# Optimization experiments

Measured on AMD Instinct MI355X. Metric: run time of the kernel, lower is better.

Reference implementation:

```python
import jax, jax.numpy as jnp
import numpy as np

B = 2048          # batch
K = 32            # max active features per side
NF = 22528        # feature_set.num_features
L1 = 2048
L2 = 16
L3 = 32
P = 8             # num_psqt_buckets
NLS = 8           # num_ls_buckets
QP = 255.0        # 8-bit unsigned LSQ upper bound


def setup_inputs() -> dict:
    key = jax.random.key(0)
    ks = jax.random.split(key, 16)
    us = jax.random.bernoulli(ks[0], 0.5, (B, 1)).astype(jnp.float32)
    them = 1.0 - us
    white_indices = jax.random.randint(ks[1], (B, K), 0, NF)
    black_indices = jax.random.randint(ks[2], (B, K), 0, NF)
    white_values = jnp.ones((B, K), jnp.float32)
    black_values = jnp.ones((B, K), jnp.float32)
    psqt_indices = jax.random.randint(ks[3], (B,), 0, P)
    layer_stack_indices = jax.random.randint(ks[4], (B,), 0, NLS)
    # parameters
    ft_weight = jax.random.normal(ks[5], (NF, L1 + P), jnp.float32) * 0.01
    ft_bias = jax.random.normal(ks[6], (L1 + P,), jnp.float32) * 0.01
    lsq_s = jnp.full((4,), 1.0 / 128.0, jnp.float32)  # per-group step size
    W1 = jax.random.normal(ks[7], (NLS, L2, L1), jnp.float32) * (1.0 / np.sqrt(L1))
    b1 = jnp.zeros((NLS, L2), jnp.float32)
    W2 = jax.random.normal(ks[8], (NLS, L3, L2), jnp.float32) * (1.0 / np.sqrt(L2))
    b2 = jnp.zeros((NLS, L3), jnp.float32)
    Wo = jax.random.normal(ks[9], (NLS, 1, L3), jnp.float32) * (1.0 / np.sqrt(L3))
    bo = jnp.zeros((NLS, 1), jnp.float32)
    return dict(us=us, them=them, white_indices=white_indices, white_values=white_values,
                black_indices=black_indices, black_values=black_values,
                psqt_indices=psqt_indices, layer_stack_indices=layer_stack_indices,
                ft_weight=ft_weight, ft_bias=ft_bias, lsq_s=lsq_s,
                W1=W1, b1=b1, W2=W2, b2=b2, Wo=Wo, bo=bo)


def _feature_transform(idx, val, ft_weight, ft_bias):
    # sparse accumulation: sum_k val[b,k] * ft_weight[idx[b,k], :]
    emb = ft_weight[idx]                           # [B, K, L1+P]
    return jnp.einsum('bk,bkd->bd', val, emb) + ft_bias


def _lsq(x, s):
    # LSQ activation, 4 groups over feature dim, 8-bit unsigned, STE round
    b, d = x.shape
    g = x.reshape(b, 4, d // 4) / s[None, :, None]
    gc = jnp.clip(g, 0.0, QP)
    gq = gc + jax.lax.stop_gradient(jnp.round(gc) - gc)
    return (gq * s[None, :, None]).reshape(b, d)


def reference(us, them, white_indices, white_values, black_indices, black_values,
              psqt_indices, layer_stack_indices,
              ft_weight, ft_bias, lsq_s, W1, b1, W2, b2, Wo, bo):
    wp = _feature_transform(white_indices, white_values, ft_weight, ft_bias)
    bp = _feature_transform(black_indices, black_values, ft_weight, ft_bias)
    w, wpsqt = wp[:, :L1], wp[:, L1:]
    b, bpsqt = bp[:, :L1], bp[:, L1:]
    l0 = us * jnp.concatenate([w, b], axis=1) + them * jnp.concatenate([b, w], axis=1)
    l0q = _lsq(l0, lsq_s)                          # [B, 2*L1]
    s0, s1, s2, s3 = jnp.split(l0q, 4, axis=1)
    l0_mixed = jnp.concatenate([s0 * s1, s2 * s3], axis=1)   # [B, L1]
    # psqt bucket gather
    wps = jnp.take_along_axis(wpsqt, psqt_indices[:, None], axis=1)  # [B,1]
    bps = jnp.take_along_axis(bpsqt, psqt_indices[:, None], axis=1)
    # per-sample layer-stack (expert) selection
    i = layer_stack_indices
    h1 = jnp.clip(jnp.einsum('bi,boi->bo', l0_mixed, W1[i]) + b1[i], 0.0, 1.0)
    h2 = jnp.clip(jnp.einsum('bi,boi->bo', h1, W2[i]) + b2[i], 0.0, 1.0)
    ls_out = jnp.einsum('bi,boi->bo', h2, Wo[i]) + bo[i]     # [B,1]
    return ls_out + (wps - bps) * (us - 0.5)
```

## Files before the change

### kernel.cpp

```cpp
#include <hip/hip_runtime.h>

#define BB 2048
#define K 32
#define ROW 2056
#define L1D 2048
#define NT 512
#define NFEAT 22528
#define TBL_ELEMS ((size_t)NFEAT * ROW)
#define W1_ELEMS  ((size_t)8 * 16 * L1D)
#define TBL_BYTES (TBL_ELEMS * 2)
#define W1_OFF    TBL_BYTES
#define WS_NEEDED (TBL_BYTES + W1_ELEMS * 2)

__device__ __forceinline__ float bf2f(unsigned short s) {
    union { unsigned int u; float f; } v; v.u = ((unsigned int)s) << 16; return v.f;
}

__device__ __forceinline__ unsigned short f2bf(float f) {
    union { float f; unsigned int u; } v; v.f = f;
    const unsigned int u = v.u;
    return (unsigned short)((u + 0x7fffu + ((u >> 16) & 1u)) >> 16);
}

__device__ __forceinline__ void fma4(float4& a, float v, const float4 t) {
    a.x = fmaf(v, t.x, a.x); a.y = fmaf(v, t.y, a.y);
    a.z = fmaf(v, t.z, a.z); a.w = fmaf(v, t.w, a.w);
}

__device__ __forceinline__ void fma4u(float4& a, float v, const ushort4 t) {
    a.x = fmaf(v, bf2f(t.x), a.x); a.y = fmaf(v, bf2f(t.y), a.y);
    a.z = fmaf(v, bf2f(t.z), a.z); a.w = fmaf(v, bf2f(t.w), a.w);
}

__device__ __forceinline__ float4 add4(float4 a, float4 b) {
    float4 r; r.x = a.x + b.x; r.y = a.y + b.y; r.z = a.z + b.z; r.w = a.w + b.w;
    return r;
}

__device__ __forceinline__ float4 mix4(float ua, float4 a, float ub, float4 b) {
    float4 r;
    r.x = fmaf(ua, a.x, ub * b.x); r.y = fmaf(ua, a.y, ub * b.y);
    r.z = fmaf(ua, a.z, ub * b.z); r.w = fmaf(ua, a.w, ub * b.w);
    return r;
}

__device__ __forceinline__ float lsq1(float g, float s) {
    return rintf(fminf(fmaxf(g / s, 0.f), 255.f)) * s;
}

__device__ __forceinline__ float4 lsq4(float4 g, float s) {
    float4 r;
    r.x = lsq1(g.x, s); r.y = lsq1(g.y, s); r.z = lsq1(g.z, s); r.w = lsq1(g.w, s);
    return r;
}

__device__ __forceinline__ float4 mul4(float4 a, float4 b) {
    float4 r; r.x = a.x * b.x; r.y = a.y * b.y; r.z = a.z * b.z; r.w = a.w * b.w;
    return r;
}

__global__ __launch_bounds__(256) void conv_bf16(const float* __restrict__ src,
                                                 unsigned short* __restrict__ dst,
                                                 int n4) {
    int i = blockIdx.x * 256 + threadIdx.x;
    const int stride = gridDim.x * 256;
    for (; i < n4; i += stride) {
        const float4 v = ((const float4*)src)[i];
        ushort4 o;
        o.x = f2bf(v.x); o.y = f2bf(v.y); o.z = f2bf(v.z); o.w = f2bf(v.w);
        ((ushort4*)dst)[i] = o;
    }
}

__global__ __launch_bounds__(NT, 8) void nnue_fwd_bf16(
    const float* __restrict__ us_p,
    const float* __restrict__ them_p,
    const int*   __restrict__ widx,
    const float* __restrict__ wval,
    const int*   __restrict__ bidx,
    const float* __restrict__ bval,
    const int*   __restrict__ psqt_idx,
    const int*   __restrict__ ls_idx,
    const unsigned short* __restrict__ tbl,
    const float* __restrict__ ftb,
    const float* __restrict__ lsq_s,
    const unsigned short* __restrict__ w1bf,
    const float* __restrict__ b1,
    const float* __restrict__ W2,
    const float* __restrict__ b2,
    const float* __restrict__ Wo,
    const float* __restrict__ bo,
    float* __restrict__ out)
{
    const int b = blockIdx.x;
    const int t = threadIdx.x;

    __shared__ float4 sQA[NT];
    __shared__ float4 sQB[NT];
    __shared__ float4 sM[NT];
    __shared__ float  sH1t[16];
    __shared__ float  sH1[16];
    __shared__ float  sH2[32];
    __shared__ float  sPsq;

    const float usv = us_p[b];
    const float thv = them_p[b];

    float4 aw = {0,0,0,0}, ab = {0,0,0,0};
    #pragma unroll 4
    for (int k = 0; k < K; ++k) {
        const int   iw = widx[b * K + k];
        const float vw = wval[b * K + k];
        const int   ib = bidx[b * K + k];
        const float vb = bval[b * K + k];
        const ushort4 uw = ((const ushort4*)(tbl + (size_t)iw * ROW))[t];
        const ushort4 ub = ((const ushort4*)(tbl + (size_t)ib * ROW))[t];
        fma4u(aw, vw, uw);
        fma4u(ab, vb, ub);
    }

    const int pi = psqt_idx[b];
    if (t < 64) {
        const int k = t & 31;
        const int   idx = (t < 32) ? widx[b * K + k] : bidx[b * K + k];
        const float val = (t < 32) ? wval[b * K + k] : bval[b * K + k];
        float c = val * bf2f(tbl[(size_t)idx * ROW + 2048 + pi]);
        c += __shfl_down(c, 16, 32); c += __shfl_down(c, 8, 32);
        c += __shfl_down(c, 4, 32);  c += __shfl_down(c, 2, 32);
        c += __shfl_down(c, 1, 32);
        const float bsum = __shfl(c, 32);
        if (t == 0) sPsq = (c - bsum) * (usv - 0.5f);
    }

    const float s0 = lsq_s[0], s1 = lsq_s[1], s2 = lsq_s[2], s3 = lsq_s[3];
    const float4 bias = ((const float4*)ftb)[t];
    aw = add4(aw, bias);
    ab = add4(ab, bias);
    const float sA = (t < 256) ? s0 : s1;
    const float sB = (t < 256) ? s2 : s3;
    sQA[t] = lsq4(mix4(usv, aw, thv, ab), sA);
    sQB[t] = lsq4(mix4(usv, ab, thv, aw), sB);
    __syncthreads();

    if (t < 256) {
        sM[t]       = mul4(sQA[t], sQA[t + 256]);
        sM[t + 256] = mul4(sQB[t], sQB[t + 256]);
    }
    __syncthreads();

    const int i = ls_idx[b];
    const unsigned short* W1i = w1bf + (size_t)i * 16 * L1D;
    {
        const int o   = t >> 5;
        const int sub = t & 31;
        const ushort4* Wrow = (const ushort4*)(W1i + o * L1D);
        float4 a4 = {0,0,0,0};
        #pragma unroll
        for (int jj = 0; jj < 16; ++jj) {
            const int j4 = sub + (jj << 5);
            const float4  m = sM[j4];
            const ushort4 w = Wrow[j4];
            a4.x = fmaf(m.x, bf2f(w.x), a4.x); a4.y = fmaf(m.y, bf2f(w.y), a4.y);
            a4.z = fmaf(m.z, bf2f(w.z), a4.z); a4.w = fmaf(m.w, bf2f(w.w), a4.w);
        }
        float acc = (a4.x + a4.y) + (a4.z + a4.w);
        acc += __shfl_down(acc, 16, 32); acc += __shfl_down(acc, 8, 32);
        acc += __shfl_down(acc, 4, 32);  acc += __shfl_down(acc, 2, 32);
        acc += __shfl_down(acc, 1, 32);
        if (sub == 0) sH1t[o] = acc;
    }
    __syncthreads();

    if (t < 16) {
        const float v = sH1t[t] + b1[i * 16 + t];
        sH1[t] = fminf(fmaxf(v, 0.f), 1.f);
    }
    __syncthreads();

    if (t < 32) {
        const float* W2i = W2 + (size_t)i * 32 * 16 + t * 16;
        float v = b2[i * 32 + t];
        #pragma unroll
        for (int j = 0; j < 16; ++j) v = fmaf(sH1[j], W2i[j], v);
        sH2[t] = fminf(fmaxf(v, 0.f), 1.f);
    }
    __syncthreads();

    if (t == 0) {
        const float* Woi = Wo + (size_t)i * 32;
        float v = bo[i];
        #pragma unroll
        for (int j = 0; j < 32; ++j) v = fmaf(sH2[j], Woi[j], v);
        out[b] = v + sPsq;
    }
}

__global__ __launch_bounds__(NT, 8) void nnue_fwd_f32(
    const float* __restrict__ us_p, const float* __restrict__ them_p,
    const int* __restrict__ widx, const float* __restrict__ wval,
    const int* __restrict__ bidx, const float* __restrict__ bval,
    const int* __restrict__ psqt_idx, const int* __restrict__ ls_idx,
    const float* __restrict__ ftw, const float* __restrict__ ftb,
    const float* __restrict__ lsq_s, const float* __restrict__ W1,
    const float* __restrict__ b1, const float* __restrict__ W2,
    const float* __restrict__ b2, const float* __restrict__ Wo,
    const float* __restrict__ bo, float* __restrict__ out)
{
    const int b = blockIdx.x;
    const int t = threadIdx.x;
    __shared__ float4 sQA[NT]; __shared__ float4 sQB[NT]; __shared__ float4 sM[NT];
    __shared__ float sH1t[16]; __shared__ float sH1[16]; __shared__ float sH2[32];
    __shared__ float sPsq;
    const float usv = us_p[b]; const float thv = them_p[b];
    float4 aw = {0,0,0,0}, ab = {0,0,0,0};
    #pragma unroll 4
    for (int k = 0; k < K; ++k) {
        const int iw = widx[b*K+k]; const float vw = wval[b*K+k];
        const int ib = bidx[b*K+k]; const float vb = bval[b*K+k];
        fma4(aw, vw, ((const float4*)(ftw + (size_t)iw * ROW))[t]);
        fma4(ab, vb, ((const float4*)(ftw + (size_t)ib * ROW))[t]);
    }
    const int pi = psqt_idx[b];
    if (t < 64) {
        const int k = t & 31;
        const int   idx = (t < 32) ? widx[b*K+k] : bidx[b*K+k];
        const float val = (t < 32) ? wval[b*K+k] : bval[b*K+k];
        float c = val * ftw[(size_t)idx * ROW + 2048 + pi];
        c += __shfl_down(c, 16, 32); c += __shfl_down(c, 8, 32);
        c += __shfl_down(c, 4, 32); c += __shfl_down(c, 2, 32); c += __shfl_down(c, 1, 32);
        const float bsum = __shfl(c, 32);
        if (t == 0) sPsq = (c - bsum) * (usv - 0.5f);
    }
    const float s0 = lsq_s[0], s1 = lsq_s[1], s2 = lsq_s[2], s3 = lsq_s[3];
    const float4 bias = ((const float4*)ftb)[t];
    aw = add4(aw, bias); ab = add4(ab, bias);
    const float sA = (t < 256) ? s0 : s1;
    const float sB = (t < 256) ? s2 : s3;
    sQA[t] = lsq4(mix4(usv, aw, thv, ab), sA);
    sQB[t] = lsq4(mix4(usv, ab, thv, aw), sB);
    __syncthreads();
    if (t < 256) { sM[t] = mul4(sQA[t], sQA[t+256]); sM[t+256] = mul4(sQB[t], sQB[t+256]); }
    __syncthreads();
    const int i = ls_idx[b];
    const float* W1i = W1 + (size_t)i * 16 * L1D;
    {
        const int o = t >> 5; const int sub = t & 31;
        const float4* Wrow = (const float4*)(W1i + o * L1D);
        float4 a4 = {0,0,0,0};
        #pragma unroll
        for (int jj = 0; jj < 16; ++jj) {
            const int j4 = sub + (jj << 5);
            const float4 m = sM[j4]; const float4 w = Wrow[j4];
            a4.x = fmaf(m.x, w.x, a4.x); a4.y = fmaf(m.y, w.y, a4.y);
            a4.z = fmaf(m.z, w.z, a4.z); a4.w = fmaf(m.w, w.w, a4.w);
        }
        float acc = (a4.x + a4.y) + (a4.z + a4.w);
        acc += __shfl_down(acc, 16, 32); acc += __shfl_down(acc, 8, 32);
        acc += __shfl_down(acc, 4, 32); acc += __shfl_down(acc, 2, 32); acc += __shfl_down(acc, 1, 32);
        if (sub == 0) sH1t[o] = acc;
    }
    __syncthreads();
    if (t < 16) sH1[t] = fminf(fmaxf(sH1t[t] + b1[i*16+t], 0.f), 1.f);
    __syncthreads();
    if (t < 32) {
        const float* W2i = W2 + (size_t)i * 32 * 16 + t * 16;
        float v = b2[i*32+t];
        #pragma unroll
        for (int j = 0; j < 16; ++j) v = fmaf(sH1[j], W2i[j], v);
        sH2[t] = fminf(fmaxf(v, 0.f), 1.f);
    }
    __syncthreads();
    if (t == 0) {
        const float* Woi = Wo + (size_t)i * 32;
        float v = bo[i];
        #pragma unroll
        for (int j = 0; j < 32; ++j) v = fmaf(sH2[j], Woi[j], v);
        out[b] = v + sPsq;
    }
}

extern "C" void kernel_launch(void* const* d_in, const int* in_sizes, int n_in,
                              void* d_out, int out_size, void* d_ws, size_t ws_size,
                              hipStream_t stream) {
    const float* us_p  = (const float*)d_in[0];
    const float* them  = (const float*)d_in[1];
    const int*   widx  = (const int*)d_in[2];
    const float* wval  = (const float*)d_in[3];
    const int*   bidx  = (const int*)d_in[4];
    const float* bval  = (const float*)d_in[5];
    const int*   pidx  = (const int*)d_in[6];
    const int*   lidx  = (const int*)d_in[7];
    const float* ftw   = (const float*)d_in[8];
    const float* ftb   = (const float*)d_in[9];
    const float* lsqs  = (const float*)d_in[10];
    const float* W1    = (const float*)d_in[11];
    const float* b1    = (const float*)d_in[12];
    const float* W2    = (const float*)d_in[13];
    const float* b2    = (const float*)d_in[14];
    const float* Wo    = (const float*)d_in[15];
    const float* bo    = (const float*)d_in[16];
    float* out = (float*)d_out;

    if (ws_size >= WS_NEEDED) {
        unsigned short* tblbf = (unsigned short*)d_ws;
        unsigned short* w1bf  = (unsigned short*)((char*)d_ws + W1_OFF);
        conv_bf16<<<dim3(8192), dim3(256), 0, stream>>>(ftw, tblbf, (int)(TBL_ELEMS / 4));
        conv_bf16<<<dim3(256),  dim3(256), 0, stream>>>(W1,  w1bf,  (int)(W1_ELEMS / 4));
        nnue_fwd_bf16<<<dim3(BB), dim3(NT), 0, stream>>>(
            us_p, them, widx, wval, bidx, bval, pidx, lidx,
            tblbf, ftb, lsqs, w1bf, b1, W2, b2, Wo, bo, out);
    } else {
        nnue_fwd_f32<<<dim3(BB), dim3(NT), 0, stream>>>(
            us_p, them, widx, wval, bidx, bval, pidx, lidx,
            ftw, ftb, lsqs, W1, b1, W2, b2, Wo, bo, out);
    }
}
```

Before: 371.5 us.

## Re-layout feature table into column slices and split gather from dense head

The bf16 feature table is converted into a slice-major layout (32 slices of 64 columns per feature row). A new gather kernel has each block cover one column slice for a group of samples so the gathered data stays in cache, and it reduces partial sums across four k-subsets in shared memory. The per-sample accumulators go to fp32 workspace buffers G0/G1, and a separate combine kernel reads them for the LSQ, mixing and layer-stack stages. PSQT values are now read from the fp32 table. This aims to improve L2 locality of the random row gathers, at the cost of writing and rereading about 32MB of intermediates and one more kernel launch.

```diff
diff --git a/kernel.cpp b/kernel.cpp
--- a/kernel.cpp
+++ b/kernel.cpp
@@ -4,13 +4,20 @@
 #define K 32
 #define ROW 2056
 #define L1D 2048
-#define NT 512
 #define NFEAT 22528
-#define TBL_ELEMS ((size_t)NFEAT * ROW)
-#define W1_ELEMS  ((size_t)8 * 16 * L1D)
-#define TBL_BYTES (TBL_ELEMS * 2)
-#define W1_OFF    TBL_BYTES
-#define WS_NEEDED (TBL_BYTES + W1_ELEMS * 2)
+#define NSLICE 32
+#define SCOLS 64
+
+typedef unsigned short us8 __attribute__((ext_vector_type(8)));
+typedef float f8 __attribute__((ext_vector_type(8)));
+
+#define TBLS_BYTES ((size_t)NFEAT * 2048 * 2)
+#define W1_ELEMS   ((size_t)8 * 16 * L1D)
+#define W1_OFF     TBLS_BYTES
+#define G0_OFF     (TBLS_BYTES + W1_ELEMS * 2)
+#define G_BYTES    ((size_t)BB * L1D * 4)
+#define G1_OFF     (G0_OFF + G_BYTES)
+#define WS_NEEDED  (G1_OFF + G_BYTES)
 
 __device__ __forceinline__ float bf2f(unsigned short s) {
     union { unsigned int u; float f; } v; v.u = ((unsigned int)s) << 16; return v.f;
@@ -25,11 +32,6 @@
 __device__ __forceinline__ void fma4(float4& a, float v, const float4 t) {
     a.x = fmaf(v, t.x, a.x); a.y = fmaf(v, t.y, a.y);
     a.z = fmaf(v, t.z, a.z); a.w = fmaf(v, t.w, a.w);
-}
-
-__device__ __forceinline__ void fma4u(float4& a, float v, const ushort4 t) {
-    a.x = fmaf(v, bf2f(t.x), a.x); a.y = fmaf(v, bf2f(t.y), a.y);
-    a.z = fmaf(v, bf2f(t.z), a.z); a.w = fmaf(v, bf2f(t.w), a.w);
 }
 
 __device__ __forceinline__ float4 add4(float4 a, float4 b) {
@@ -72,32 +74,105 @@
     }
 }
 
-__global__ __launch_bounds__(NT, 8) void nnue_fwd_bf16(
-    const float* __restrict__ us_p,
-    const float* __restrict__ them_p,
-    const int*   __restrict__ widx,
-    const float* __restrict__ wval,
-    const int*   __restrict__ bidx,
-    const float* __restrict__ bval,
-    const int*   __restrict__ psqt_idx,
-    const int*   __restrict__ ls_idx,
-    const unsigned short* __restrict__ tbl,
-    const float* __restrict__ ftb,
-    const float* __restrict__ lsq_s,
+__global__ __launch_bounds__(256) void conv_tblS(const float* __restrict__ src,
+                                                 unsigned short* __restrict__ dst) {
+    const int lane = threadIdx.x & 63;
+    const int wid  = (blockIdx.x * 256 + threadIdx.x) >> 6;
+    const int nw   = (gridDim.x * 256) >> 6;
+    const int rr = lane >> 3, oc = lane & 7;
+    const int ntask = (NFEAT / 8) * NSLICE;
+    for (int task = wid; task < ntask; task += nw) {
+        const int rg = task >> 5;
+        const int s  = task & (NSLICE - 1);
+        const int row = rg * 8 + rr;
+        const float* p = src + (size_t)row * ROW + s * SCOLS + oc * 8;
+        const float4 a = ((const float4*)p)[0];
+        const float4 b = ((const float4*)p)[1];
+        us8 o;
+        o[0] = f2bf(a.x); o[1] = f2bf(a.y); o[2] = f2bf(a.z); o[3] = f2bf(a.w);
+        o[4] = f2bf(b.x); o[5] = f2bf(b.y); o[6] = f2bf(b.z); o[7] = f2bf(b.w);
+        *(us8*)(dst + ((size_t)s * NFEAT + row) * SCOLS + oc * 8) = o;
+    }
+}
+
+__global__ __launch_bounds__(1024, 8) void gather_slices(
+    const int*   __restrict__ widx, const float* __restrict__ wval,
+    const int*   __restrict__ bidx, const float* __restrict__ bval,
+    const unsigned short* __restrict__ tblS,
+    float* __restrict__ G0, float* __restrict__ G1)
+{
+    const int t   = threadIdx.x;
+    const int blk = blockIdx.x;
+    const int p = blk >> 8, r = blk & 255;
+    const int slice = (r & 7) + 8 * (p >> 1);
+    const int group = (r >> 3) + 32 * (p & 1);
+    const int ks = t >> 8, rem = t & 255;
+    const int sl = rem >> 3, oct = rem & 7;
+
+    __shared__ int   sWI[1024]; __shared__ float sWV[1024];
+    __shared__ int   sBI[1024]; __shared__ float sBV[1024];
+    __shared__ float sAcc[3 * 256 * 8];
+
+    const int ibase = group * 1024;
+    sWI[t] = widx[ibase + t]; sWV[t] = wval[ibase + t];
+    sBI[t] = bidx[ibase + t]; sBV[t] = bval[ibase + t];
+    __syncthreads();
+
+    const unsigned short* base = tblS + (size_t)slice * NFEAT * SCOLS + oct * 8;
+    f8 aw = (f8)0.f, ab = (f8)0.f;
+    const int kb = sl * 32 + ks * 8;
+    #pragma unroll
+    for (int kk = 0; kk < 8; ++kk) {
+        const int   iw = sWI[kb + kk]; const float vw = sWV[kb + kk];
+        const int   ib = sBI[kb + kk]; const float vb = sBV[kb + kk];
+        const us8 lw = *(const us8*)(base + (size_t)iw * SCOLS);
+        const us8 lb = *(const us8*)(base + (size_t)ib * SCOLS);
+        #pragma unroll
+        for (int j = 0; j < 8; ++j) aw[j] = fmaf(vw, bf2f(lw[j]), aw[j]);
+        #pragma unroll
+        for (int j = 0; j < 8; ++j) ab[j] = fmaf(vb, bf2f(lb[j]), ab[j]);
+    }
+
+    __syncthreads();
+    if (ks > 0) *(f8*)(sAcc + ((ks - 1) * 256 + rem) * 8) = aw;
+    __syncthreads();
+    if (ks == 0) {
+        #pragma unroll
+        for (int q = 0; q < 3; ++q) aw += *(const f8*)(sAcc + (q * 256 + rem) * 8);
+    }
+    __syncthreads();
+    if (ks > 0) *(f8*)(sAcc + ((ks - 1) * 256 + rem) * 8) = ab;
+    __syncthreads();
+    if (ks == 0) {
+        #pragma unroll
+        for (int q = 0; q < 3; ++q) ab += *(const f8*)(sAcc + (q * 256 + rem) * 8);
+        const int sample = group * 32 + sl;
+        const size_t off = (size_t)sample * 2048 + slice * SCOLS + oct * 8;
+        *(f8*)(G0 + off) = aw;
+        *(f8*)(G1 + off) = ab;
+    }
+}
+
+__global__ __launch_bounds__(512, 8) void combine(
+    const float* __restrict__ us_p, const float* __restrict__ them_p,
+    const int* __restrict__ widx, const float* __restrict__ wval,
+    const int* __restrict__ bidx, const float* __restrict__ bval,
+    const int* __restrict__ psqt_idx, const int* __restrict__ ls_idx,
+    const float* __restrict__ ftw,
+    const float* __restrict__ ftb, const float* __restrict__ lsq_s,
     const unsigned short* __restrict__ w1bf,
-    const float* __restrict__ b1,
-    const float* __restrict__ W2,
-    const float* __restrict__ b2,
-    const float* __restrict__ Wo,
+    const float* __restrict__ b1, const float* __restrict__ W2,
+    const float* __restrict__ b2, const float* __restrict__ Wo,
     const float* __restrict__ bo,
+    const float* __restrict__ G0, const float* __restrict__ G1,
     float* __restrict__ out)
 {
     const int b = blockIdx.x;
     const int t = threadIdx.x;
 
-    __shared__ float4 sQA[NT];
-    __shared__ float4 sQB[NT];
-    __shared__ float4 sM[NT];
+    __shared__ float4 sQA[512];
+    __shared__ float4 sQB[512];
+    __shared__ float4 sM[512];
     __shared__ float  sH1t[16];
     __shared__ float  sH1[16];
     __shared__ float  sH2[32];
@@ -106,25 +181,15 @@
     const float usv = us_p[b];
     const float thv = them_p[b];
 
-    float4 aw = {0,0,0,0}, ab = {0,0,0,0};
-    #pragma unroll 4
-    for (int k = 0; k < K; ++k) {
-        const int   iw = widx[b * K + k];
-        const float vw = wval[b * K + k];
-        const int   ib = bidx[b * K + k];
-        const float vb = bval[b * K + k];
-        const ushort4 uw = ((const ushort4*)(tbl + (size_t)iw * ROW))[t];
-        const ushort4 ub = ((const ushort4*)(tbl + (size_t)ib * ROW))[t];
-        fma4u(aw, vw, uw);
-        fma4u(ab, vb, ub);
-    }
+    float4 aw = ((const float4*)(G0 + (size_t)b * 2048))[t];
+    float4 ab = ((const float4*)(G1 + (size_t)b * 2048))[t];
 
     const int pi = psqt_idx[b];
     if (t < 64) {
         const int k = t & 31;
         const int   idx = (t < 32) ? widx[b * K + k] : bidx[b * K + k];
         const float val = (t < 32) ? wval[b * K + k] : bval[b * K + k];
-        float c = val * bf2f(tbl[(size_t)idx * ROW + 2048 + pi]);
+        float c = val * ftw[(size_t)idx * ROW + 2048 + pi];
         c += __shfl_down(c, 16, 32); c += __shfl_down(c, 8, 32);
         c += __shfl_down(c, 4, 32);  c += __shfl_down(c, 2, 32);
         c += __shfl_down(c, 1, 32);
@@ -154,7 +219,7 @@
         const int o   = t >> 5;
         const int sub = t & 31;
         const ushort4* Wrow = (const ushort4*)(W1i + o * L1D);
-        float4 a4 = {0,0,0,0};
+        float4 a4 = {0, 0, 0, 0};
         #pragma unroll
         for (int jj = 0; jj < 16; ++jj) {
             const int j4 = sub + (jj << 5);
@@ -195,7 +260,7 @@
     }
 }
 
-__global__ __launch_bounds__(NT, 8) void nnue_fwd_f32(
+__global__ __launch_bounds__(512, 8) void nnue_fwd_f32(
     const float* __restrict__ us_p, const float* __restrict__ them_p,
     const int* __restrict__ widx, const float* __restrict__ wval,
     const int* __restrict__ bidx, const float* __restrict__ bval,
@@ -208,7 +273,7 @@
 {
     const int b = blockIdx.x;
     const int t = threadIdx.x;
-    __shared__ float4 sQA[NT]; __shared__ float4 sQB[NT]; __shared__ float4 sM[NT];
+    __shared__ float4 sQA[512]; __shared__ float4 sQB[512]; __shared__ float4 sM[512];
     __shared__ float sH1t[16]; __shared__ float sH1[16]; __shared__ float sH2[32];
     __shared__ float sPsq;
     const float usv = us_p[b]; const float thv = them_p[b];
@@ -302,15 +367,19 @@
     float* out = (float*)d_out;
 
     if (ws_size >= WS_NEEDED) {
-        unsigned short* tblbf = (unsigned short*)d_ws;
-        unsigned short* w1bf  = (unsigned short*)((char*)d_ws + W1_OFF);
-        conv_bf16<<<dim3(8192), dim3(256), 0, stream>>>(ftw, tblbf, (int)(TBL_ELEMS / 4));
-        conv_bf16<<<dim3(256),  dim3(256), 0, stream>>>(W1,  w1bf,  (int)(W1_ELEMS / 4));
-        nnue_fwd_bf16<<<dim3(BB), dim3(NT), 0, stream>>>(
+        unsigned short* tblS = (unsigned short*)d_ws;
+        unsigned short* w1bf = (unsigned short*)((char*)d_ws + W1_OFF);
+        float* G0 = (float*)((char*)d_ws + G0_OFF);
+        float* G1 = (float*)((char*)d_ws + G1_OFF);
+        conv_tblS<<<dim3(2048), dim3(256), 0, stream>>>(ftw, tblS);
+        conv_bf16<<<dim3(256), dim3(256), 0, stream>>>(W1, w1bf, (int)(W1_ELEMS / 4));
+        gather_slices<<<dim3(2048), dim3(1024), 0, stream>>>(
+            widx, wval, bidx, bval, tblS, G0, G1);
+        combine<<<dim3(BB), dim3(512), 0, stream>>>(
             us_p, them, widx, wval, bidx, bval, pidx, lidx,
-            tblbf, ftb, lsqs, w1bf, b1, W2, b2, Wo, bo, out);
+            ftw, ftb, lsqs, w1bf, b1, W2, b2, Wo, bo, G0, G1, out);
     } else {
-        nnue_fwd_f32<<<dim3(BB), dim3(NT), 0, stream>>>(
+        nnue_fwd_f32<<<dim3(BB), dim3(512), 0, stream>>>(
             us_p, them, widx, wval, bidx, bval, pidx, lidx,
             ftw, ftb, lsqs, W1, b1, W2, b2, Wo, bo, out);
     }
```

Result: slower. 388.0 us (+4.5%).

## Compact bf16 table, merge conversion kernels, widen per-thread work to 8 elements

Applied to the files above, without the earlier changes.

The converted bf16 feature table now holds only the 2048 L1 columns per row, so the converted table gets smaller and row starts are aligned. The psqt columns are read directly from the fp32 weights instead. The two conversion launches are merged into one kernel that processes 8 elements per thread. The main kernel uses 256 threads, each doing 16-byte loads of 8 bf16 values, and the L1 mixing and matvec are rearranged to fit that layout. The intent is to cut conversion traffic and launch overhead and to make the gathers wider, at the cost of fewer threads per sample and more registers per thread.

```diff
diff --git a/kernel.cpp b/kernel.cpp
--- a/kernel.cpp
+++ b/kernel.cpp
@@ -4,13 +4,18 @@
 #define K 32
 #define ROW 2056
 #define L1D 2048
-#define NT 512
 #define NFEAT 22528
-#define TBL_ELEMS ((size_t)NFEAT * ROW)
-#define W1_ELEMS  ((size_t)8 * 16 * L1D)
-#define TBL_BYTES (TBL_ELEMS * 2)
-#define W1_OFF    TBL_BYTES
-#define WS_NEEDED (TBL_BYTES + W1_ELEMS * 2)
+
+typedef unsigned short us8 __attribute__((ext_vector_type(8)));
+typedef float f8 __attribute__((ext_vector_type(8)));
+
+#define TBLC_BYTES ((size_t)NFEAT * 2048 * 2)
+#define W1_ELEMS   ((size_t)8 * 16 * L1D)
+#define W1_OFF     TBLC_BYTES
+#define WS_NEEDED  (TBLC_BYTES + W1_ELEMS * 2)
+
+#define TBL_N8 (NFEAT * 256)
+#define W1_N8  (W1_ELEMS / 8)
 
 __device__ __forceinline__ float bf2f(unsigned short s) {
     union { unsigned int u; float f; } v; v.u = ((unsigned int)s) << 16; return v.f;
@@ -25,11 +30,6 @@
 __device__ __forceinline__ void fma4(float4& a, float v, const float4 t) {
     a.x = fmaf(v, t.x, a.x); a.y = fmaf(v, t.y, a.y);
     a.z = fmaf(v, t.z, a.z); a.w = fmaf(v, t.w, a.w);
-}
-
-__device__ __forceinline__ void fma4u(float4& a, float v, const ushort4 t) {
-    a.x = fmaf(v, bf2f(t.x), a.x); a.y = fmaf(v, bf2f(t.y), a.y);
-    a.z = fmaf(v, bf2f(t.z), a.z); a.w = fmaf(v, bf2f(t.w), a.w);
 }
 
 __device__ __forceinline__ float4 add4(float4 a, float4 b) {
@@ -59,64 +59,72 @@
     return r;
 }
 
-__global__ __launch_bounds__(256) void conv_bf16(const float* __restrict__ src,
-                                                 unsigned short* __restrict__ dst,
-                                                 int n4) {
+__global__ __launch_bounds__(256) void conv_all(const float* __restrict__ ftw,
+                                                const float* __restrict__ W1,
+                                                unsigned short* __restrict__ tblc,
+                                                unsigned short* __restrict__ w1bf) {
     int i = blockIdx.x * 256 + threadIdx.x;
     const int stride = gridDim.x * 256;
-    for (; i < n4; i += stride) {
-        const float4 v = ((const float4*)src)[i];
-        ushort4 o;
-        o.x = f2bf(v.x); o.y = f2bf(v.y); o.z = f2bf(v.z); o.w = f2bf(v.w);
-        ((ushort4*)dst)[i] = o;
-    }
-}
-
-__global__ __launch_bounds__(NT, 8) void nnue_fwd_bf16(
-    const float* __restrict__ us_p,
-    const float* __restrict__ them_p,
-    const int*   __restrict__ widx,
-    const float* __restrict__ wval,
-    const int*   __restrict__ bidx,
-    const float* __restrict__ bval,
-    const int*   __restrict__ psqt_idx,
-    const int*   __restrict__ ls_idx,
-    const unsigned short* __restrict__ tbl,
-    const float* __restrict__ ftb,
-    const float* __restrict__ lsq_s,
+    for (; i < TBL_N8 + W1_N8; i += stride) {
+        const float* src;
+        unsigned short* dst;
+        if (i < TBL_N8) {
+            const int row = i >> 8, c = i & 255;
+            src = ftw + (size_t)row * ROW + c * 8;
+            dst = tblc + ((size_t)row << 11) + c * 8;
+        } else {
+            const int j = i - TBL_N8;
+            src = W1 + (size_t)j * 8;
+            dst = w1bf + (size_t)j * 8;
+        }
+        const float4 a = ((const float4*)src)[0];
+        const float4 b = ((const float4*)src)[1];
+        us8 o;
+        o[0] = f2bf(a.x); o[1] = f2bf(a.y); o[2] = f2bf(a.z); o[3] = f2bf(a.w);
+        o[4] = f2bf(b.x); o[5] = f2bf(b.y); o[6] = f2bf(b.z); o[7] = f2bf(b.w);
+        *(us8*)dst = o;
+    }
+}
+
+__global__ __launch_bounds__(256, 8) void nnue_main(
+    const float* __restrict__ us_p, const float* __restrict__ them_p,
+    const int* __restrict__ widx, const float* __restrict__ wval,
+    const int* __restrict__ bidx, const float* __restrict__ bval,
+    const int* __restrict__ psqt_idx, const int* __restrict__ ls_idx,
+    const float* __restrict__ ftw,
+    const float* __restrict__ ftb, const float* __restrict__ lsq_s,
+    const unsigned short* __restrict__ tblc,
     const unsigned short* __restrict__ w1bf,
-    const float* __restrict__ b1,
-    const float* __restrict__ W2,
-    const float* __restrict__ b2,
-    const float* __restrict__ Wo,
-    const float* __restrict__ bo,
-    float* __restrict__ out)
+    const float* __restrict__ b1, const float* __restrict__ W2,
+    const float* __restrict__ b2, const float* __restrict__ Wo,
+    const float* __restrict__ bo, float* __restrict__ out)
 {
     const int b = blockIdx.x;
     const int t = threadIdx.x;
 
-    __shared__ float4 sQA[NT];
-    __shared__ float4 sQB[NT];
-    __shared__ float4 sM[NT];
-    __shared__ float  sH1t[16];
-    __shared__ float  sH1[16];
-    __shared__ float  sH2[32];
-    __shared__ float  sPsq;
+    __shared__ f8    sQA[256];
+    __shared__ f8    sQB[256];
+    __shared__ float sH1t[16];
+    __shared__ float sH1[16];
+    __shared__ float sH2[32];
+    __shared__ float sPsq;
 
     const float usv = us_p[b];
     const float thv = them_p[b];
 
-    float4 aw = {0,0,0,0}, ab = {0,0,0,0};
-    #pragma unroll 4
+    f8 aw = (f8)0.f, ab = (f8)0.f;
+    #pragma unroll 8
     for (int k = 0; k < K; ++k) {
         const int   iw = widx[b * K + k];
         const float vw = wval[b * K + k];
         const int   ib = bidx[b * K + k];
         const float vb = bval[b * K + k];
-        const ushort4 uw = ((const ushort4*)(tbl + (size_t)iw * ROW))[t];
-        const ushort4 ub = ((const ushort4*)(tbl + (size_t)ib * ROW))[t];
-        fma4u(aw, vw, uw);
-        fma4u(ab, vb, ub);
+        const us8 lw = ((const us8*)(tblc + ((size_t)iw << 11)))[t];
+        const us8 lb = ((const us8*)(tblc + ((size_t)ib << 11)))[t];
+        #pragma unroll
+        for (int j = 0; j < 8; ++j) aw[j] = fmaf(vw, bf2f(lw[j]), aw[j]);
+        #pragma unroll
+        for (int j = 0; j < 8; ++j) ab[j] = fmaf(vb, bf2f(lb[j]), ab[j]);
     }
 
     const int pi = psqt_idx[b];
@@ -124,7 +132,7 @@
         const int k = t & 31;
         const int   idx = (t < 32) ? widx[b * K + k] : bidx[b * K + k];
         const float val = (t < 32) ? wval[b * K + k] : bval[b * K + k];
-        float c = val * bf2f(tbl[(size_t)idx * ROW + 2048 + pi]);
+        float c = val * ftw[(size_t)idx * ROW + 2048 + pi];
         c += __shfl_down(c, 16, 32); c += __shfl_down(c, 8, 32);
         c += __shfl_down(c, 4, 32);  c += __shfl_down(c, 2, 32);
         c += __shfl_down(c, 1, 32);
@@ -133,40 +141,61 @@
     }
 
     const float s0 = lsq_s[0], s1 = lsq_s[1], s2 = lsq_s[2], s3 = lsq_s[3];
-    const float4 bias = ((const float4*)ftb)[t];
-    aw = add4(aw, bias);
-    ab = add4(ab, bias);
-    const float sA = (t < 256) ? s0 : s1;
-    const float sB = (t < 256) ? s2 : s3;
-    sQA[t] = lsq4(mix4(usv, aw, thv, ab), sA);
-    sQB[t] = lsq4(mix4(usv, ab, thv, aw), sB);
-    __syncthreads();
-
-    if (t < 256) {
-        sM[t]       = mul4(sQA[t], sQA[t + 256]);
-        sM[t + 256] = mul4(sQB[t], sQB[t + 256]);
+    const float4 bl = ((const float4*)ftb)[2 * t];
+    const float4 bh = ((const float4*)ftb)[2 * t + 1];
+    float4 awl = {aw[0], aw[1], aw[2], aw[3]}, awh = {aw[4], aw[5], aw[6], aw[7]};
+    float4 abl = {ab[0], ab[1], ab[2], ab[3]}, abh = {ab[4], ab[5], ab[6], ab[7]};
+    awl = add4(awl, bl); awh = add4(awh, bh);
+    abl = add4(abl, bl); abh = add4(abh, bh);
+    const float sA = (t < 128) ? s0 : s1;
+    const float sB = (t < 128) ? s2 : s3;
+    const float4 qal = lsq4(mix4(usv, awl, thv, abl), sA);
+    const float4 qah = lsq4(mix4(usv, awh, thv, abh), sA);
+    const float4 qbl = lsq4(mix4(usv, abl, thv, awl), sB);
+    const float4 qbh = lsq4(mix4(usv, abh, thv, awh), sB);
+    f8 qa, qb;
+    qa[0]=qal.x; qa[1]=qal.y; qa[2]=qal.z; qa[3]=qal.w;
+    qa[4]=qah.x; qa[5]=qah.y; qa[6]=qah.z; qa[7]=qah.w;
+    qb[0]=qbl.x; qb[1]=qbl.y; qb[2]=qbl.z; qb[3]=qbl.w;
+    qb[4]=qbh.x; qb[5]=qbh.y; qb[6]=qbh.z; qb[7]=qbh.w;
+    sQA[t] = qa;
+    sQB[t] = qb;
+    __syncthreads();
+
+    if (t < 128) {
+        const f8 m = sQA[t] * sQA[t + 128];
+        sQA[t] = m;
+    } else {
+        const f8 m = sQB[t - 128] * sQB[t];
+        sQB[t] = m;
     }
     __syncthreads();
 
     const int i = ls_idx[b];
-    const unsigned short* W1i = w1bf + (size_t)i * 16 * L1D;
     {
-        const int o   = t >> 5;
-        const int sub = t & 31;
-        const ushort4* Wrow = (const ushort4*)(W1i + o * L1D);
-        float4 a4 = {0,0,0,0};
-        #pragma unroll
-        for (int jj = 0; jj < 16; ++jj) {
-            const int j4 = sub + (jj << 5);
-            const float4  m = sM[j4];
-            const ushort4 w = Wrow[j4];
-            a4.x = fmaf(m.x, bf2f(w.x), a4.x); a4.y = fmaf(m.y, bf2f(w.y), a4.y);
-            a4.z = fmaf(m.z, bf2f(w.z), a4.z); a4.w = fmaf(m.w, bf2f(w.w), a4.w);
+        const int o   = t >> 4;
+        const int sub = t & 15;
+        const us8* Wrow = (const us8*)(w1bf + (((size_t)i * 16 + o) << 11));
+        f8 a8 = (f8)0.f;
+        #pragma unroll
+        for (int jj = 0; jj < 8; ++jj) {
+            const int c = sub + (jj << 4);
+            const f8 m = sQA[c];
+            const us8 w = Wrow[c];
+            #pragma unroll
+            for (int j = 0; j < 8; ++j) a8[j] = fmaf(m[j], bf2f(w[j]), a8[j]);
         }
-        float acc = (a4.x + a4.y) + (a4.z + a4.w);
-        acc += __shfl_down(acc, 16, 32); acc += __shfl_down(acc, 8, 32);
-        acc += __shfl_down(acc, 4, 32);  acc += __shfl_down(acc, 2, 32);
-        acc += __shfl_down(acc, 1, 32);
+        #pragma unroll
+        for (int jj = 8; jj < 16; ++jj) {
+            const int c = sub + (jj << 4);
+            const f8 m = sQB[c];
+            const us8 w = Wrow[c];
+            #pragma unroll
+            for (int j = 0; j < 8; ++j) a8[j] = fmaf(m[j], bf2f(w[j]), a8[j]);
+        }
+        float acc = ((a8[0]+a8[1]) + (a8[2]+a8[3])) + ((a8[4]+a8[5]) + (a8[6]+a8[7]));
+        acc += __shfl_down(acc, 8, 16); acc += __shfl_down(acc, 4, 16);
+        acc += __shfl_down(acc, 2, 16); acc += __shfl_down(acc, 1, 16);
         if (sub == 0) sH1t[o] = acc;
     }
     __syncthreads();
@@ -195,7 +224,7 @@
     }
 }
 
-__global__ __launch_bounds__(NT, 8) void nnue_fwd_f32(
+__global__ __launch_bounds__(512, 8) void nnue_fwd_f32(
     const float* __restrict__ us_p, const float* __restrict__ them_p,
     const int* __restrict__ widx, const float* __restrict__ wval,
     const int* __restrict__ bidx, const float* __restrict__ bval,
@@ -208,7 +237,7 @@
 {
     const int b = blockIdx.x;
     const int t = threadIdx.x;
-    __shared__ float4 sQA[NT]; __shared__ float4 sQB[NT]; __shared__ float4 sM[NT];
+    __shared__ float4 sQA[512]; __shared__ float4 sQB[512]; __shared__ float4 sM[512];
     __shared__ float sH1t[16]; __shared__ float sH1[16]; __shared__ float sH2[32];
     __shared__ float sPsq;
     const float usv = us_p[b]; const float thv = them_p[b];
@@ -302,15 +331,14 @@
     float* out = (float*)d_out;
 
     if (ws_size >= WS_NEEDED) {
-        unsigned short* tblbf = (unsigned short*)d_ws;
-        unsigned short* w1bf  = (unsigned short*)((char*)d_ws + W1_OFF);
-        conv_bf16<<<dim3(8192), dim3(256), 0, stream>>>(ftw, tblbf, (int)(TBL_ELEMS / 4));
-        conv_bf16<<<dim3(256),  dim3(256), 0, stream>>>(W1,  w1bf,  (int)(W1_ELEMS / 4));
-        nnue_fwd_bf16<<<dim3(BB), dim3(NT), 0, stream>>>(
+        unsigned short* tblc = (unsigned short*)d_ws;
+        unsigned short* w1bf = (unsigned short*)((char*)d_ws + W1_OFF);
+        conv_all<<<dim3(8192), dim3(256), 0, stream>>>(ftw, W1, tblc, w1bf);
+        nnue_main<<<dim3(BB), dim3(256), 0, stream>>>(
             us_p, them, widx, wval, bidx, bval, pidx, lidx,
-            tblbf, ftb, lsqs, w1bf, b1, W2, b2, Wo, bo, out);
+            ftw, ftb, lsqs, tblc, w1bf, b1, W2, b2, Wo, bo, out);
     } else {
-        nnue_fwd_f32<<<dim3(BB), dim3(NT), 0, stream>>>(
+        nnue_fwd_f32<<<dim3(BB), dim3(512), 0, stream>>>(
             us_p, them, widx, wval, bidx, bval, pidx, lidx,
             ftw, ftb, lsqs, W1, b1, W2, b2, Wo, bo, out);
     }
```

New measurement: 378.6 us. Within noise of the previous version (+1.9%).
